# Optimization experiments

Measured on AMD Instinct MI355X. Metric: run time of the kernel, lower is better.

Reference implementation:

```python
import jax, jax.numpy as jnp
import numpy as np

D_MODEL, D_STATE, EXPAND = 256, 16, 2
D_INNER = EXPAND * D_MODEL
DT_RANK = (D_MODEL + 15) // 16
BATCH, SEQLEN = 4, 4096


def silu(x):
    return x * jax.nn.sigmoid(x)


def setup_inputs() -> dict:
    key = jax.random.key(0)
    ks = jax.random.split(key, 10)
    h = jax.random.normal(ks[0], (BATCH, SEQLEN, D_MODEL), dtype=jnp.float32)
    Wi_f = jax.random.normal(ks[1], (2 * D_INNER, D_MODEL), dtype=jnp.float32) / np.sqrt(D_MODEL)
    Wi_b = jax.random.normal(ks[2], (2 * D_INNER, D_MODEL), dtype=jnp.float32) / np.sqrt(D_MODEL)
    Wx_f = jax.random.normal(ks[3], (DT_RANK + 2 * D_STATE, D_INNER), dtype=jnp.float32) / np.sqrt(D_INNER)
    Wx_b = jax.random.normal(ks[4], (DT_RANK + 2 * D_STATE, D_INNER), dtype=jnp.float32) / np.sqrt(D_INNER)
    dt_std = DT_RANK ** -0.5
    Wdt_f = jax.random.uniform(ks[5], (D_INNER, DT_RANK), dtype=jnp.float32, minval=-dt_std, maxval=dt_std)
    Wdt_b = jax.random.uniform(ks[6], (D_INNER, DT_RANK), dtype=jnp.float32, minval=-dt_std, maxval=dt_std)
    # dt bias = inverse-softplus of dt sampled log-uniform in [1e-3, 1e-1]
    dt = jnp.exp(jax.random.uniform(ks[7], (D_INNER,), dtype=jnp.float32) * (np.log(0.1) - np.log(0.001)) + np.log(0.001))
    dt = jnp.clip(dt, 1e-4, None)
    inv_dt = dt + jnp.log(-jnp.expm1(-dt))
    bdt_f = inv_dt
    bdt_b = inv_dt
    A_log = jnp.log(jnp.broadcast_to(jnp.arange(1, D_STATE + 1, dtype=jnp.float32), (D_INNER, D_STATE)))
    A_log_f = A_log
    A_log_b = A_log
    D_f = jnp.ones((D_INNER,), dtype=jnp.float32)
    D_b = jnp.ones((D_INNER,), dtype=jnp.float32)
    Wo = jax.random.normal(ks[8], (D_MODEL, 2 * D_INNER), dtype=jnp.float32) / np.sqrt(2 * D_INNER)
    return {"hidden_states": h, "Wi_f": Wi_f, "Wi_b": Wi_b, "Wx_f": Wx_f, "Wx_b": Wx_b,
            "Wdt_f": Wdt_f, "Wdt_b": Wdt_b, "bdt_f": bdt_f, "bdt_b": bdt_b,
            "A_log_f": A_log_f, "A_log_b": A_log_b, "D_f": D_f, "D_b": D_b, "Wo": Wo}


def mamba_dir(h, Wi, Wx, Wdt, bdt, A_log, Dp, reverse):
    b, l, _ = h.shape
    di, r = Wdt.shape
    n = A_log.shape[1]
    xz = h @ Wi.T                      # [b,l,2*di]
    if reverse:
        xz = xz[:, ::-1]
    x, z = xz[..., :di], xz[..., di:]
    u = silu(x)                        # selective_scan input u
    x_dbl = u @ Wx.T                   # [b,l,r+2n]
    delta = jax.nn.softplus(x_dbl[..., :r] @ Wdt.T + bdt)   # [b,l,di]
    Bm = x_dbl[..., r:r + n]           # [b,l,n]
    Cm = x_dbl[..., r + n:r + 2 * n]   # [b,l,n]
    A = -jnp.exp(A_log)                # [di,n]

    def step(s, inp):
        u_t, d_t, B_t, C_t = inp       # [b,di],[b,di],[b,n],[b,n]
        dA = jnp.exp(d_t[..., None] * A)                         # [b,di,n]
        s = dA * s + (d_t * u_t)[..., None] * B_t[:, None, :]    # [b,di,n]
        y_t = jnp.einsum('bdn,bn->bd', s, C_t)
        return s, y_t

    s0 = jnp.zeros((b, di, n), dtype=u.dtype)
    xs = (jnp.swapaxes(u, 0, 1), jnp.swapaxes(delta, 0, 1),
          jnp.swapaxes(Bm, 0, 1), jnp.swapaxes(Cm, 0, 1))
    _, ys = jax.lax.scan(step, s0, xs)
    y = jnp.swapaxes(ys, 0, 1) + u * Dp          # skip term D*u
    y = y * silu(z)                              # gated output
    if reverse:
        y = y[:, ::-1]
    return y


def reference(hidden_states, Wi_f, Wi_b, Wx_f, Wx_b, Wdt_f, Wdt_b, bdt_f, bdt_b, A_log_f, A_log_b, D_f, D_b, Wo):
    y_f = mamba_dir(hidden_states, Wi_f, Wx_f, Wdt_f, bdt_f, A_log_f, D_f, False)
    y_b = mamba_dir(hidden_states, Wi_b, Wx_b, Wdt_b, bdt_b, A_log_b, D_b, True)
    y = jnp.concatenate([y_f, y_b], axis=-1)     # [b,l,2*di]
    return y @ Wo.T                              # [b,l,d_model]
```

## Files before the change

### kernel.cpp

```cpp
#include <hip/hip_runtime.h>
#include <hip/hip_bf16.h>
#include <cstddef>
#include <cstdint>

#define D_MODELc 256
#define D_STATEc 16
#define D_INNERc 512
#define DT_RANKc 16
#define BATCHc   4
#define SEQLENc  4096
#define NCHUNK   128
#define CHUNK    32

typedef unsigned short u16;
typedef __attribute__((ext_vector_type(8))) short bf16x8;
typedef __attribute__((ext_vector_type(4))) float f32x4;
typedef float __attribute__((ext_vector_type(4))) f4v;
typedef __attribute__((ext_vector_type(4))) uint32_t u32x4;

#define VMCNT8() asm volatile("s_waitcnt vmcnt(8)" ::: "memory")
#define VMCNT0() asm volatile("s_waitcnt vmcnt(0)" ::: "memory")

__device__ __forceinline__ float siluf(float v) { return v / (1.f + __expf(-v)); }

__device__ __forceinline__ u16 bf16_rne(float f) {
    uint32_t u = __float_as_uint(f);
    u += 0x7fffu + ((u >> 16) & 1u);
    return (u16)(u >> 16);
}
__device__ __forceinline__ float bf16_to_f(u16 h) {
    return __uint_as_float(((uint32_t)h) << 16);
}
__device__ __forceinline__ uint32_t pack_hl(float f) {
    u16 hh = bf16_rne(f);
    u16 ll = bf16_rne(f - bf16_to_f(hh));
    return ((uint32_t)hh << 16) | ll;
}
__device__ __forceinline__ float unpack_add(uint32_t v) {
    return __uint_as_float(v & 0xFFFF0000u) + __uint_as_float(v << 16);
}
__device__ __forceinline__ void unpack_frag(const uint32_t* q, bf16x8& fh, bf16x8& fl) {
    union { bf16x8 v; uint32_t w[4]; } H, L;
    #pragma unroll
    for (int i = 0; i < 4; i++) {
        uint32_t a = q[2 * i], b = q[2 * i + 1];
        H.w[i] = (a >> 16) | (b & 0xFFFF0000u);
        L.w[i] = (a & 0xFFFFu) | (b << 16);
    }
    fh = H.v; fl = L.v;
}
__device__ __forceinline__ float softplusf(float x) {
    return fmaxf(x, 0.f) + __logf(1.f + __expf(-fabsf(x)));
}
__device__ __forceinline__ float dot16_tree(const f4v x[4], const float* w, float bias) {
    float t0 = fmaf(x[0][1], w[1],  x[0][0] * w[0]);
    float t1 = fmaf(x[0][3], w[3],  x[0][2] * w[2]);
    float t2 = fmaf(x[1][1], w[5],  x[1][0] * w[4]);
    float t3 = fmaf(x[1][3], w[7],  x[1][2] * w[6]);
    float t4 = fmaf(x[2][1], w[9],  x[2][0] * w[8]);
    float t5 = fmaf(x[2][3], w[11], x[2][2] * w[10]);
    float t6 = fmaf(x[3][1], w[13], x[3][0] * w[12]);
    float t7 = fmaf(x[3][3], w[15], x[3][2] * w[14]);
    return bias + (((t0 + t1) + (t2 + t3)) + ((t4 + t5) + (t6 + t7)));
}
__device__ __forceinline__ void qladder(float q, float* qd) {
    float q2 = q * q;
    float q4 = q2 * q2;
    float q8 = q4 * q4;
    qd[0] = q;        qd[1] = q2;       qd[2] = q2 * q;     qd[3] = q4;
    qd[4] = q4 * q;   qd[5] = q4 * q2;  qd[6] = q4 * qd[2]; qd[7] = q8;
    qd[8] = q8 * q;   qd[9] = q8 * q2;  qd[10] = q8 * qd[2]; qd[11] = q8 * q4;
    qd[12] = q8 * qd[4]; qd[13] = q8 * qd[5]; qd[14] = q8 * qd[6]; qd[15] = q8 * q8;
}

#define GLL16(g, l) __builtin_amdgcn_global_load_lds( \
    (const __attribute__((address_space(1))) uint32_t*)(g), \
    (__attribute__((address_space(3))) uint32_t*)(l), 16, 0, 0)

__global__ __launch_bounds__(256) void split5_kernel(
        const float* __restrict__ s0, const float* __restrict__ s1,
        const float* __restrict__ s2, const float* __restrict__ s3,
        const float* __restrict__ s4,
        u16* __restrict__ h0, u16* __restrict__ l0,
        u16* __restrict__ h1, u16* __restrict__ l1,
        u16* __restrict__ h2, u16* __restrict__ l2,
        u16* __restrict__ h3, u16* __restrict__ l3,
        u16* __restrict__ h4, u16* __restrict__ l4,
        int n4w, int n4x) {
    const int which = blockIdx.y;
    const float* in; u16* hi; u16* lo; int n4;
    if      (which == 0) { in = s0; hi = h0; lo = l0; n4 = n4w; }
    else if (which == 1) { in = s1; hi = h1; lo = l1; n4 = n4w; }
    else if (which == 2) { in = s2; hi = h2; lo = l2; n4 = n4w; }
    else if (which == 3) { in = s3; hi = h3; lo = l3; n4 = n4x; }
    else                 { in = s4; hi = h4; lo = l4; n4 = n4x; }
    for (int i = blockIdx.x * 256 + threadIdx.x; i < n4; i += gridDim.x * 256) {
        float4 v = ((const float4*)in)[i];
        u16 a0 = bf16_rne(v.x), a1 = bf16_rne(v.y), a2 = bf16_rne(v.z), a3 = bf16_rne(v.w);
        ushort4 hv; hv.x = a0; hv.y = a1; hv.z = a2; hv.w = a3;
        ushort4 lv;
        lv.x = bf16_rne(v.x - bf16_to_f(a0));
        lv.y = bf16_rne(v.y - bf16_to_f(a1));
        lv.z = bf16_rne(v.z - bf16_to_f(a2));
        lv.w = bf16_rne(v.w - bf16_to_f(a3));
        ((ushort4*)hi)[i] = hv;
        ((ushort4*)lo)[i] = lv;
    }
}

__global__ __launch_bounds__(256) void split_kernel(const float* __restrict__ in,
                                                    u16* __restrict__ hi,
                                                    u16* __restrict__ lo, int n4) {
    int i = blockIdx.x * 256 + threadIdx.x;
    const int stride = gridDim.x * 256;
    for (; i < n4; i += stride) {
        float4 v = ((const float4*)in)[i];
        u16 a0 = bf16_rne(v.x), a1 = bf16_rne(v.y), a2 = bf16_rne(v.z), a3 = bf16_rne(v.w);
        ushort4 hv; hv.x = a0; hv.y = a1; hv.z = a2; hv.w = a3;
        ushort4 lv;
        lv.x = bf16_rne(v.x - bf16_to_f(a0));
        lv.y = bf16_rne(v.y - bf16_to_f(a1));
        lv.z = bf16_rne(v.z - bf16_to_f(a2));
        lv.w = bf16_rne(v.w - bf16_to_f(a3));
        ((ushort4*)hi)[i] = hv;
        ((ushort4*)lo)[i] = lv;
    }
}

template<int EPI, int NBL2, int AINT>
__global__ __launch_bounds__(256) void gemm_mfma(
        const u16* __restrict__ Ah, const u16* __restrict__ Al, int lda,
        const u16* __restrict__ Bh, const u16* __restrict__ Bl, int ldb,
        float* __restrict__ out0,
        uint32_t* __restrict__ uhl,
        int M, int N, int K) {
    __shared__ char lds[2][32768];
    const int t    = threadIdx.x;
    const int lane = t & 63;
    const int wid  = t >> 6;
    const int wrow = wid >> 1, wcol = wid & 1;

    const int id  = blockIdx.x;
    const int xcd = id & 7;
    const int j   = id >> 3;
    const int nb  = j & ((1 << NBL2) - 1);
    const int mg  = j >> NBL2;
    const int m0  = (mg * 8 + xcd) * 128;
    const int n0  = nb * 128;

    const int lr  = lane & 15;
    const int kgl = lane >> 4;

    f32x4 acc[4][4] = {};

    const char* gp[8];
    if (AINT == 0) {
        #pragma unroll
        for (int i = 0; i < 8; i++) {
            int c    = i * 256 + t;
            int tile = c >> 9;
            int kg   = (c >> 7) & 3;
            int row  = c & 127;
            const u16* bsrc = (tile == 0) ? Ah : (tile == 1) ? Al : (tile == 2) ? Bh : Bl;
            int r0 = (tile < 2) ? m0 : n0;
            int ld = (tile < 2) ? lda : ldb;
            gp[i] = (const char*)(bsrc + (size_t)(r0 + row) * ld + kg * 8);
        }
    } else {
        #pragma unroll
        for (int i = 0; i < 4; i++) {
            int c    = i * 256 + t;
            int kg   = c >> 8;
            int row  = (c >> 1) & 127;
            int half = c & 1;
            gp[i] = (const char*)((const uint32_t*)Ah + (size_t)(m0 + row) * lda + kg * 8 + half * 4);
        }
        #pragma unroll
        for (int i = 4; i < 8; i++) {
            int cb   = (i - 4) * 256 + t;
            int tile = cb >> 9;
            int kg   = (cb >> 7) & 3;
            int row  = cb & 127;
            const u16* bsrc = tile ? Bl : Bh;
            gp[i] = (const char*)(bsrc + (size_t)(n0 + row) * ldb + kg * 8);
        }
    }
    const int ldst_t = t << 4;

    auto stage = [&](int buf) {
        #pragma unroll
        for (int i = 0; i < 8; i++) {
            GLL16(gp[i], ((char*)lds) + buf * 32768 + i * 4096 + ldst_t);
            gp[i] += (AINT == 1 && i < 4) ? 128 : 64;
        }
    };

    const int NT = K >> 5;
    stage(0);
    if (NT > 1) stage(1);

    for (int kt = 0; kt < NT; ++kt) {
        const int buf = kt & 1;
        if (kt + 1 < NT) { VMCNT8(); } else { VMCNT0(); }
        __builtin_amdgcn_sched_barrier(0);
        __builtin_amdgcn_s_barrier();
        __builtin_amdgcn_sched_barrier(0);

        bf16x8 afh[4], afl[4];
        if (AINT == 0) {
            const u16* lb = (const u16*)lds[buf];
            #pragma unroll
            for (int mi = 0; mi < 4; mi++) {
                int row = wrow * 64 + mi * 16 + lr;
                afh[mi] = *(const bf16x8*)(lb + 0 * 4096 + kgl * 1024 + row * 8);
                afl[mi] = *(const bf16x8*)(lb + 1 * 4096 + kgl * 1024 + row * 8);
            }
        } else {
            const uint32_t* la = (const uint32_t*)lds[buf];
            #pragma unroll
            for (int mi = 0; mi < 4; mi++) {
                int row = wrow * 64 + mi * 16 + lr;
                unpack_frag(la + kgl * 1024 + row * 8, afh[mi], afl[mi]);
            }
        }
        const u16* lbB = (const u16*)(lds[buf] + 16384);
        #pragma unroll
        for (int ni = 0; ni < 4; ni++) {
            int row = wcol * 64 + ni * 16 + lr;
            bf16x8 bfh = *(const bf16x8*)(lbB + 0 * 4096 + kgl * 1024 + row * 8);
            bf16x8 bfl = *(const bf16x8*)(lbB + 1 * 4096 + kgl * 1024 + row * 8);
            #pragma unroll
            for (int mi = 0; mi < 4; mi++) {
                acc[mi][ni] = __builtin_amdgcn_mfma_f32_16x16x32_bf16(afh[mi], bfh, acc[mi][ni], 0, 0, 0);
                acc[mi][ni] = __builtin_amdgcn_mfma_f32_16x16x32_bf16(afh[mi], bfl, acc[mi][ni], 0, 0, 0);
                acc[mi][ni] = __builtin_amdgcn_mfma_f32_16x16x32_bf16(afl[mi], bfh, acc[mi][ni], 0, 0, 0);
            }
        }
        __builtin_amdgcn_sched_barrier(0);
        __builtin_amdgcn_s_barrier();
        __builtin_amdgcn_sched_barrier(0);
        if (kt + 2 < NT) stage(buf);
    }

    uint32_t* lds32 = (uint32_t*)lds;
    {
        const int dirn = (EPI == 1) ? (nb >> 3) : 0;
        const bool is_u = (EPI == 1) && (((nb >> 2) & 1) == 0);
        #pragma unroll
        for (int mi = 0; mi < 4; mi++) {
            #pragma unroll
            for (int ni = 0; ni < 4; ni++) {
                #pragma unroll
                for (int r = 0; r < 4; r++) {
                    int row = wrow * 64 + mi * 16 + kgl * 4 + r;
                    int col = wcol * 64 + ni * 16 + lr;
                    int swz = ((row >> 2) & 3) << 4;
                    float v = acc[mi][ni][r];
                    uint32_t w;
                    if (EPI == 0) w = __float_as_uint(v);
                    else {
                        float s = siluf(v);
                        w = is_u ? pack_hl(s) : __float_as_uint(s);
                    }
                    lds32[row * 128 + (col ^ swz)] = w;
                }
            }
        }
        __syncthreads();
        if (EPI == 0) {
            float* base = out0 + (size_t)m0 * N + n0;
            #pragma unroll
            for (int i = 0; i < 16; i++) {
                int idx = i * 256 + t;
                int row = idx >> 5, c4 = idx & 31;
                int swz = ((row >> 2) & 3) << 4;
                f4v v = *(const f4v*)(lds32 + row * 128 + ((c4 * 4) ^ swz));
                __builtin_nontemporal_store(v, (f4v*)(base + (size_t)row * N + c4 * 4));
            }
        } else {
            const int colbase = (nb & 3) * 128;
            if (is_u) {
                uint32_t* base = uhl + (size_t)dirn * M * 512 + (size_t)m0 * 512 + colbase;
                #pragma unroll
                for (int i = 0; i < 16; i++) {
                    int idx = i * 256 + t;
                    int row = idx >> 5, c4 = idx & 31;
                    int swz = ((row >> 2) & 3) << 4;
                    *(u32x4*)(base + (size_t)row * 512 + c4 * 4) =
                        *(const u32x4*)(lds32 + row * 128 + ((c4 * 4) ^ swz));
                }
            } else {
                float* base = out0 + (size_t)m0 * 1024 + (size_t)dirn * 512 + colbase;
                #pragma unroll
                for (int i = 0; i < 16; i++) {
                    int idx = i * 256 + t;
                    int row = idx >> 5, c4 = idx & 31;
                    int swz = ((row >> 2) & 3) << 4;
                    *(f4v*)(base + (size_t)row * 1024 + c4 * 4) =
                        *(const f4v*)(lds32 + row * 128 + ((c4 * 4) ^ swz));
                }
            }
        }
    }
}

__global__ __launch_bounds__(256) void xdbl_mfma(
        const uint32_t* __restrict__ Uhl,
        const u16* __restrict__ WxH, const u16* __restrict__ WxL,
        float* __restrict__ out) {
    __shared__ uint32_t lds[4][64][8];
    const int t    = threadIdx.x;
    const int lane = t & 63;
    const int wid  = t >> 6;
    const int m0   = blockIdx.x * 64;
    const int dir  = blockIdx.y;
    const int Mp   = gridDim.x * 64;
    const int lr   = lane & 15;
    const int kgl  = lane >> 4;

    const size_t dofU = (size_t)dir * (size_t)Mp * 512;
    const size_t dofW = (size_t)dir * (size_t)48 * 512;

    const char* gp[2];
    #pragma unroll
    for (int i = 0; i < 2; i++) {
        int c    = i * 256 + t;
        int kg   = c >> 7;
        int row  = (c >> 1) & 63;
        int half = c & 1;
        gp[i] = (const char*)(Uhl + dofU + (size_t)(m0 + row) * 512 + kg * 8 + half * 4);
    }
    const int ldst_t = t << 4;

    f32x4 acc[3] = {};

    for (int k0 = 0; k0 < 512; k0 += 32) {
        #pragma unroll
        for (int i = 0; i < 2; i++) {
            GLL16(gp[i], ((char*)lds) + i * 4096 + ldst_t);
            gp[i] += 128;
        }
        __syncthreads();

        bf16x8 afh, afl;
        unpack_frag(&lds[kgl][wid * 16 + lr][0], afh, afl);
        #pragma unroll
        for (int nf = 0; nf < 3; nf++) {
            const size_t boff = dofW + (size_t)(nf * 16 + lr) * 512 + k0 + kgl * 8;
            bf16x8 bfh = *(const bf16x8*)(WxH + boff);
            bf16x8 bfl = *(const bf16x8*)(WxL + boff);
            acc[nf] = __builtin_amdgcn_mfma_f32_16x16x32_bf16(afh, bfh, acc[nf], 0, 0, 0);
            acc[nf] = __builtin_amdgcn_mfma_f32_16x16x32_bf16(afh, bfl, acc[nf], 0, 0, 0);
            acc[nf] = __builtin_amdgcn_mfma_f32_16x16x32_bf16(afl, bfh, acc[nf], 0, 0, 0);
        }
        __syncthreads();
    }

    float* o = out + (size_t)dir * (size_t)Mp * 48;
    #pragma unroll
    for (int nf = 0; nf < 3; nf++) {
        #pragma unroll
        for (int r = 0; r < 4; r++) {
            int m = m0 + wid * 16 + kgl * 4 + r;
            int n = nf * 16 + lr;
            o[(size_t)m * 48 + n] = acc[nf][r];
        }
    }
}

__global__ __launch_bounds__(256) void scan_phaseA(
        const uint32_t* __restrict__ Uhl,
        const float* __restrict__ XD,
        const float* __restrict__ Wdt_f, const float* __restrict__ Wdt_b,
        const float* __restrict__ bdt_f, const float* __restrict__ bdt_b,
        const float* __restrict__ AL_f, const float* __restrict__ AL_b,
        float* __restrict__ SDL, float* __restrict__ S) {
    const int c   = blockIdx.x;
    const int d   = blockIdx.y * 256 + threadIdx.x;
    const int z   = blockIdx.z;
    const int dir = z & 1;
    const int b   = z >> 1;
    const int PB  = gridDim.z >> 1;
    const int Mp  = PB * SEQLENc;
    const float* Wdt = dir ? Wdt_b : Wdt_f;
    const float* bdt = dir ? bdt_b : bdt_f;
    const float* AL  = dir ? AL_b  : AL_f;
    const uint32_t* UD = Uhl + (size_t)dir * Mp * 512;
    const float* XDD = XD + (size_t)dir * Mp * 48;

    float w[16], a[16], s[16];
    #pragma unroll
    for (int n = 0; n < 16; n++) {
        w[n] = Wdt[d * 16 + n];
        a[n] = -__expf(AL[d * 16 + n]);
        s[n] = 0.f;
    }
    const float a0 = a[0];
    bool pw = (a0 != 0.f);
    #pragma unroll
    for (int n = 1; n < 16; n++)
        pw = pw && (fabsf(a[n] - (float)(n + 1) * a0) <= 3e-6f * fabsf(a[n]));
    const float bb = bdt[d];
    float sdl = 0.f;

    for (int i = 0; i < CHUNK; i++) {
        int tt = c * CHUNK + i;
        int l  = dir ? (SEQLENc - 1 - tt) : tt;
        size_t row = (size_t)b * SEQLENc + l;
        float uu = unpack_add(UD[row * 512 + d]);
        const f4v* xr4 = (const f4v*)&XDD[row * 48];
        f4v xw[4] = {xr4[0], xr4[1], xr4[2], xr4[3]};
        float dl = softplusf(dot16_tree(xw, w, bb));
        sdl += dl;
        float du = dl * uu;
        if (pw) {
            float qd[16];
            qladder(__expf(a0 * dl), qd);
            #pragma unroll
            for (int g = 0; g < 4; g++) {
                f4v B4 = xr4[4 + g];
                #pragma unroll
                for (int jj = 0; jj < 4; jj++) {
                    int n = g * 4 + jj;
                    s[n] = fmaf(qd[n], s[n], du * B4[jj]);
                }
            }
        } else {
            #pragma unroll
            for (int g = 0; g < 4; g++) {
                f4v B4 = xr4[4 + g];
                #pragma unroll
                for (int jj = 0; jj < 4; jj++) {
                    int n = g * 4 + jj;
                    float dA = __expf(dl * a[n]);
                    s[n] = fmaf(dA, s[n], du * B4[jj]);
                }
            }
        }
    }
    SDL[((size_t)z * NCHUNK + c) * 512 + d] = sdl;
    size_t base = (((size_t)z * NCHUNK + c) * 16) * 512 + d;
    #pragma unroll
    for (int n = 0; n < 16; n++)
        S[base + (size_t)n * 512] = s[n];
}

__global__ __launch_bounds__(256) void scan_phaseB(const float* __restrict__ SDL,
                                                   float* __restrict__ S,
                                                   const float* __restrict__ AL_f,
                                                   const float* __restrict__ AL_b) {
    const int g   = blockIdx.x * 256 + threadIdx.x;
    const int d   = g & 511;
    const int n   = (g >> 9) & 15;
    const int z   = g >> 13;
    const int dir = z & 1;
    const float an = -__expf((dir ? AL_b : AL_f)[d * 16 + n]);
    const size_t strideS = (size_t)16 * 512;
    size_t offS = (((size_t)z * NCHUNK) * 16 + n) * 512 + d;
    size_t offD = ((size_t)z * NCHUNK) * 512 + d;
    float carry = 0.f;
    float sdl = SDL[offD], ss = S[offS];
    for (int c = 0; c < NCHUNK; c++) {
        float sdn = 0.f, sn = 0.f;
        if (c + 1 < NCHUNK) { sdn = SDL[offD + 512]; sn = S[offS + strideS]; }
        float pp = __expf(an * sdl);
        S[offS] = carry;
        carry = pp * carry + ss;
        sdl = sdn; ss = sn;
        offS += strideS; offD += 512;
    }
}

__global__ __launch_bounds__(256) void scan_phaseC(
        const uint32_t* __restrict__ Uhl,
        const float* __restrict__ XD,
        const float* __restrict__ Wdt_f, const float* __restrict__ Wdt_b,
        const float* __restrict__ bdt_f, const float* __restrict__ bdt_b,
        const float* __restrict__ AL_f, const float* __restrict__ AL_b,
        const float* __restrict__ E,
        const float* SZ,
        const float* __restrict__ D_f,  const float* __restrict__ D_b,
        uint32_t* Yhl) {
    const int c   = blockIdx.x;
    const int d   = blockIdx.y * 256 + threadIdx.x;
    const int z   = blockIdx.z;
    const int dir = z & 1;
    const int b   = z >> 1;
    const int PB  = gridDim.z >> 1;
    const int Mp  = PB * SEQLENc;
    const float* Wdt = dir ? Wdt_b : Wdt_f;
    const float* bdt = dir ? bdt_b : bdt_f;
    const float* AL  = dir ? AL_b  : AL_f;
    const uint32_t* UD = Uhl + (size_t)dir * Mp * 512;
    const float* XDD = XD + (size_t)dir * Mp * 48;

    float w[16], a[16], s[16];
    size_t base = (((size_t)z * NCHUNK + c) * 16) * 512 + d;
    #pragma unroll
    for (int n = 0; n < 16; n++) {
        w[n] = Wdt[d * 16 + n];
        a[n] = -__expf(AL[d * 16 + n]);
        s[n] = E[base + (size_t)n * 512];
    }
    const float a0 = a[0];
    bool pw = (a0 != 0.f);
    #pragma unroll
    for (int n = 1; n < 16; n++)
        pw = pw && (fabsf(a[n] - (float)(n + 1) * a0) <= 3e-6f * fabsf(a[n]));
    const float bb = bdt[d];
    const float Dd = (dir ? D_b : D_f)[d];

    for (int i = 0; i < CHUNK; i++) {
        int tt = c * CHUNK + i;
        int l  = dir ? (SEQLENc - 1 - tt) : tt;
        size_t row = (size_t)b * SEQLENc + l;
        float uu = unpack_add(UD[row * 512 + d]);
        const f4v* xr4 = (const f4v*)&XDD[row * 48];
        f4v xw[4] = {xr4[0], xr4[1], xr4[2], xr4[3]};
        float dl = softplusf(dot16_tree(xw, w, bb));
        float du = dl * uu;
        float yp0 = 0.f, yp1 = 0.f, yp2 = 0.f, yp3 = 0.f;
        if (pw) {
            float qd[16];
            qladder(__expf(a0 * dl), qd);
            #pragma unroll
            for (int g = 0; g < 4; g++) {
                f4v B4 = xr4[4 + g];
                f4v C4 = xr4[8 + g];
                float yp = 0.f;
                #pragma unroll
                for (int jj = 0; jj < 4; jj++) {
                    int n = g * 4 + jj;
                    s[n] = fmaf(qd[n], s[n], du * B4[jj]);
                    yp = fmaf(s[n], C4[jj], yp);
                }
                if (g == 0) yp0 = yp; else if (g == 1) yp1 = yp;
                else if (g == 2) yp2 = yp; else yp3 = yp;
            }
        } else {
            #pragma unroll
            for (int g = 0; g < 4; g++) {
                f4v B4 = xr4[4 + g];
                f4v C4 = xr4[8 + g];
                float yp = 0.f;
                #pragma unroll
                for (int jj = 0; jj < 4; jj++) {
                    int n = g * 4 + jj;
                    float dA = __expf(dl * a[n]);
                    s[n] = fmaf(dA, s[n], du * B4[jj]);
                    yp = fmaf(s[n], C4[jj], yp);
                }
                if (g == 0) yp0 = yp; else if (g == 1) yp1 = yp;
                else if (g == 2) yp2 = yp; else yp3 = yp;
            }
        }
        float y = (yp0 + yp1) + (yp2 + yp3);
        size_t zi = row * 1024 + (size_t)dir * 512 + d;
        float sz = SZ[zi];
        float yv = (y + uu * Dd) * sz;
        Yhl[zi] = pack_hl(yv);
    }
}

extern "C" void kernel_launch(void* const* d_in, const int* in_sizes, int n_in,
                              void* d_out, int out_size, void* d_ws, size_t ws_size,
                              hipStream_t stream) {
    const float* h    = (const float*)d_in[0];
    const float* Wi_f = (const float*)d_in[1];
    const float* Wi_b = (const float*)d_in[2];
    const float* Wx_f = (const float*)d_in[3];
    const float* Wx_b = (const float*)d_in[4];
    const float* Wdt_f= (const float*)d_in[5];
    const float* Wdt_b= (const float*)d_in[6];
    const float* bdt_f= (const float*)d_in[7];
    const float* bdt_b= (const float*)d_in[8];
    const float* Al_f = (const float*)d_in[9];
    const float* Al_b = (const float*)d_in[10];
    const float* D_f  = (const float*)d_in[11];
    const float* D_b  = (const float*)d_in[12];
    const float* Wo   = (const float*)d_in[13];
    float* out = (float*)d_out;

    const size_t W_ELE  = 1024 * 256;
    const size_t WX_ELE = 48 * 512;
    const size_t FB   = (size_t)SEQLENc * D_INNERc;
    const size_t FH   = (size_t)SEQLENc * D_MODELc;
    const size_t FX   = (size_t)SEQLENc * 48;
    const size_t FP   = (size_t)NCHUNK * 16 * 512;
    const size_t FD   = (size_t)NCHUNK * 512;

    const size_t fixed_bytes = (8 * W_ELE + 4 * WX_ELE) * sizeof(u16);
    const size_t per_b = 2 * FH * sizeof(u16)
                       + 2 * FB * sizeof(float)
                       + 2 * FB * sizeof(uint32_t)
                       + 2 * FX * sizeof(float)
                       + 2 * (FP + FD) * sizeof(float);
    int PB = 4;
    if (fixed_bytes + 4 * per_b + 65536 > ws_size) PB = 2;
    if (fixed_bytes + 2 * per_b + 65536 > ws_size) PB = 1;

    char* cur = (char*)d_ws;
    auto alloc = [&](size_t bytes) -> char* {
        char* p = cur; cur += (bytes + 255) & ~(size_t)255; return p;
    };
    u16* WiH = (u16*)alloc(2 * W_ELE * 2);
    u16* WiL = (u16*)alloc(2 * W_ELE * 2);
    u16* WoH = (u16*)alloc(W_ELE * 2);
    u16* WoL = (u16*)alloc(W_ELE * 2);
    u16* WxH = (u16*)alloc(2 * WX_ELE * 2);
    u16* WxL = (u16*)alloc(2 * WX_ELE * 2);
    u16*      hH  = (u16*)alloc((size_t)PB * FH * 2);
    u16*      hL  = (u16*)alloc((size_t)PB * FH * 2);
    float*    sz  = (float*)alloc((size_t)PB * 2 * FB * 4);
    uint32_t* uhl = (uint32_t*)alloc((size_t)PB * 2 * FB * 4);
    float*    xd  = (float*)alloc((size_t)PB * 2 * FX * 4);
    float*    SDL = (float*)alloc((size_t)PB * 2 * FD * 4);
    float*    S   = (float*)alloc((size_t)PB * 2 * FP * 4);
    uint32_t* yhl = (uint32_t*)sz;

    {
        int n4w = (int)(W_ELE / 4);
        int n4x = (int)(WX_ELE / 4);
        split5_kernel<<<dim3(64, 5), 256, 0, stream>>>(
            Wi_f, Wi_b, Wo, Wx_f, Wx_b,
            WiH, WiL, WiH + W_ELE, WiL + W_ELE, WoH, WoL,
            WxH, WxL, WxH + WX_ELE, WxL + WX_ELE,
            n4w, n4x);
    }

    for (int b0 = 0; b0 < BATCHc; b0 += PB) {
        const int Mp = PB * SEQLENc;
        const int MB = Mp / 128;
        const float* hB = h   + (size_t)b0 * FH;
        float*       oB = out + (size_t)b0 * FH;

        {
            int n4 = (int)((size_t)PB * FH / 4);
            int blocks = (n4 + 255) / 256; if (blocks > 2048) blocks = 2048;
            split_kernel<<<blocks, 256, 0, stream>>>(hB, hH, hL, n4);
        }

        gemm_mfma<1, 4, 0><<<16 * MB, 256, 0, stream>>>(
            hH, hL, D_MODELc, WiH, WiL, D_MODELc,
            sz, uhl, Mp, 2048, D_MODELc);

        xdbl_mfma<<<dim3(Mp / 64, 2), 256, 0, stream>>>(uhl, WxH, WxL, xd);

        scan_phaseA<<<dim3(NCHUNK, 2, 2 * PB), 256, 0, stream>>>(
            uhl, xd, Wdt_f, Wdt_b, bdt_f, bdt_b, Al_f, Al_b, SDL, S);
        scan_phaseB<<<PB * 64, 256, 0, stream>>>(SDL, S, Al_f, Al_b);
        scan_phaseC<<<dim3(NCHUNK, 2, 2 * PB), 256, 0, stream>>>(
            uhl, xd, Wdt_f, Wdt_b, bdt_f, bdt_b, Al_f, Al_b,
            S, sz, D_f, D_b, yhl);

        gemm_mfma<0, 1, 1><<<2 * MB, 256, 0, stream>>>(
            (const u16*)yhl, nullptr, 1024, WoH, WoL, 1024,
            oB, nullptr, Mp, D_MODELc, 1024);
    }
}
```

Before: 317.5 us.

## Process two M-tiles per block in input GEMM and split-K the output GEMM

The input projection GEMM now has each block handle two consecutive 128-row M tiles with a continuous load pipeline, so the shared B (weight) tiles stay cache-hot and launch/prologue cost is amortized. The output projection GEMM is split along K into two halves to double the grid and improve occupancy. The second half writes into a new partial buffer, and an added elementwise kernel sums it into the output. This costs an extra full-output read/write pass, a second launch and a second accumulator array, which raises register pressure.

```diff
diff --git a/kernel.cpp b/kernel.cpp
--- a/kernel.cpp
+++ b/kernel.cpp
@@ -127,7 +127,18 @@
     }
 }
 
-template<int EPI, int NBL2, int AINT>
+__global__ __launch_bounds__(256) void add_kernel(float* __restrict__ out,
+                                                  const float* __restrict__ part,
+                                                  int n4) {
+    int i = blockIdx.x * 256 + threadIdx.x;
+    for (; i < n4; i += gridDim.x * 256) {
+        f4v a = ((const f4v*)out)[i];
+        f4v b = ((const f4v*)part)[i];
+        ((f4v*)out)[i] = a + b;
+    }
+}
+
+template<int EPI, int NBL2, int AINT, int MTILES, int KSPLIT>
 __global__ __launch_bounds__(256) void gemm_mfma(
         const u16* __restrict__ Ah, const u16* __restrict__ Al, int lda,
         const u16* __restrict__ Bh, const u16* __restrict__ Bl, int ldb,
@@ -144,14 +155,19 @@
     const int xcd = id & 7;
     const int j   = id >> 3;
     const int nb  = j & ((1 << NBL2) - 1);
-    const int mg  = j >> NBL2;
-    const int m0  = (mg * 8 + xcd) * 128;
+    const int jj  = j >> NBL2;
+    const int ks  = (KSPLIT == 2) ? (jj & 1) : 0;
+    const int mg  = (KSPLIT == 2) ? (jj >> 1) : jj;
+    const int m0  = (mg * 8 + xcd) * (128 * MTILES);
     const int n0  = nb * 128;
+    const int Keff  = K / KSPLIT;
+    const int kbase = ks * Keff;
 
     const int lr  = lane & 15;
     const int kgl = lane >> 4;
 
-    f32x4 acc[4][4] = {};
+    f32x4 acc0[4][4] = {};
+    f32x4 acc1[4][4] = {};
 
     const char* gp[8];
     if (AINT == 0) {
@@ -164,7 +180,7 @@
             const u16* bsrc = (tile == 0) ? Ah : (tile == 1) ? Al : (tile == 2) ? Bh : Bl;
             int r0 = (tile < 2) ? m0 : n0;
             int ld = (tile < 2) ? lda : ldb;
-            gp[i] = (const char*)(bsrc + (size_t)(r0 + row) * ld + kg * 8);
+            gp[i] = (const char*)(bsrc + (size_t)(r0 + row) * ld + kg * 8 + kbase);
         }
     } else {
         #pragma unroll
@@ -173,7 +189,7 @@
             int kg   = c >> 8;
             int row  = (c >> 1) & 127;
             int half = c & 1;
-            gp[i] = (const char*)((const uint32_t*)Ah + (size_t)(m0 + row) * lda + kg * 8 + half * 4);
+            gp[i] = (const char*)((const uint32_t*)Ah + (size_t)(m0 + row) * lda + kg * 8 + half * 4 + kbase);
         }
         #pragma unroll
         for (int i = 4; i < 8; i++) {
@@ -182,7 +198,7 @@
             int kg   = (cb >> 7) & 3;
             int row  = cb & 127;
             const u16* bsrc = tile ? Bl : Bh;
-            gp[i] = (const char*)(bsrc + (size_t)(n0 + row) * ldb + kg * 8);
+            gp[i] = (const char*)(bsrc + (size_t)(n0 + row) * ldb + kg * 8 + kbase);
         }
     }
     const int ldst_t = t << 4;
@@ -195,17 +211,7 @@
         }
     };
 
-    const int NT = K >> 5;
-    stage(0);
-    if (NT > 1) stage(1);
-
-    for (int kt = 0; kt < NT; ++kt) {
-        const int buf = kt & 1;
-        if (kt + 1 < NT) { VMCNT8(); } else { VMCNT0(); }
-        __builtin_amdgcn_sched_barrier(0);
-        __builtin_amdgcn_s_barrier();
-        __builtin_amdgcn_sched_barrier(0);
-
+    auto compute = [&](int buf, f32x4 (&acc)[4][4]) {
         bf16x8 afh[4], afl[4];
         if (AINT == 0) {
             const u16* lb = (const u16*)lds[buf];
@@ -236,14 +242,50 @@
                 acc[mi][ni] = __builtin_amdgcn_mfma_f32_16x16x32_bf16(afl[mi], bfh, acc[mi][ni], 0, 0, 0);
             }
         }
+    };
+
+    const int NT = Keff >> 5;
+    stage(0);
+    stage(1);
+
+    for (int kt = 0; kt < NT; ++kt) {
+        const int buf = kt & 1;
+        if (MTILES == 2 || kt + 1 < NT) { VMCNT8(); } else { VMCNT0(); }
         __builtin_amdgcn_sched_barrier(0);
         __builtin_amdgcn_s_barrier();
         __builtin_amdgcn_sched_barrier(0);
-        if (kt + 2 < NT) stage(buf);
-    }
-
-    uint32_t* lds32 = (uint32_t*)lds;
-    {
+        compute(buf, acc0);
+        __builtin_amdgcn_sched_barrier(0);
+        __builtin_amdgcn_s_barrier();
+        __builtin_amdgcn_sched_barrier(0);
+        int g = kt + 2;
+        if (MTILES == 2 && g == NT) {
+            if (AINT == 0) {
+                #pragma unroll
+                for (int i = 0; i < 4; i++) gp[i] += (size_t)128 * lda * 2 - (size_t)Keff * 2;
+                #pragma unroll
+                for (int i = 4; i < 8; i++) gp[i] -= (size_t)Keff * 2;
+            }
+        }
+        if (g < MTILES * NT) stage(g & 1);
+    }
+    if constexpr (MTILES == 2) {
+        for (int kt = NT; kt < 2 * NT; ++kt) {
+            const int buf = kt & 1;
+            if (kt + 1 < 2 * NT) { VMCNT8(); } else { VMCNT0(); }
+            __builtin_amdgcn_sched_barrier(0);
+            __builtin_amdgcn_s_barrier();
+            __builtin_amdgcn_sched_barrier(0);
+            compute(buf, acc1);
+            __builtin_amdgcn_sched_barrier(0);
+            __builtin_amdgcn_s_barrier();
+            __builtin_amdgcn_sched_barrier(0);
+            if (kt + 2 < 2 * NT) stage(kt & 1);
+        }
+    }
+
+    auto epilog = [&](f32x4 (&acc)[4][4], int mbase) {
+        uint32_t* lds32 = (uint32_t*)lds;
         const int dirn = (EPI == 1) ? (nb >> 3) : 0;
         const bool is_u = (EPI == 1) && (((nb >> 2) & 1) == 0);
         #pragma unroll
@@ -268,19 +310,20 @@
         }
         __syncthreads();
         if (EPI == 0) {
-            float* base = out0 + (size_t)m0 * N + n0;
+            float* obase = (KSPLIT == 2 && ks == 1) ? (float*)uhl : out0;
+            float* base = obase + (size_t)mbase * N + n0;
             #pragma unroll
             for (int i = 0; i < 16; i++) {
                 int idx = i * 256 + t;
                 int row = idx >> 5, c4 = idx & 31;
                 int swz = ((row >> 2) & 3) << 4;
-                f4v v = *(const f4v*)(lds32 + row * 128 + ((c4 * 4) ^ swz));
-                __builtin_nontemporal_store(v, (f4v*)(base + (size_t)row * N + c4 * 4));
+                *(f4v*)(base + (size_t)row * N + c4 * 4) =
+                    *(const f4v*)(lds32 + row * 128 + ((c4 * 4) ^ swz));
             }
         } else {
             const int colbase = (nb & 3) * 128;
             if (is_u) {
-                uint32_t* base = uhl + (size_t)dirn * M * 512 + (size_t)m0 * 512 + colbase;
+                uint32_t* base = uhl + (size_t)dirn * M * 512 + (size_t)mbase * 512 + colbase;
                 #pragma unroll
                 for (int i = 0; i < 16; i++) {
                     int idx = i * 256 + t;
@@ -290,7 +333,7 @@
                         *(const u32x4*)(lds32 + row * 128 + ((c4 * 4) ^ swz));
                 }
             } else {
-                float* base = out0 + (size_t)m0 * 1024 + (size_t)dirn * 512 + colbase;
+                float* base = out0 + (size_t)mbase * 1024 + (size_t)dirn * 512 + colbase;
                 #pragma unroll
                 for (int i = 0; i < 16; i++) {
                     int idx = i * 256 + t;
@@ -301,6 +344,11 @@
                 }
             }
         }
+    };
+    epilog(acc0, m0);
+    if constexpr (MTILES == 2) {
+        __syncthreads();
+        epilog(acc1, m0 + 128);
     }
 }
 
@@ -594,7 +642,8 @@
                        + 2 * FB * sizeof(float)
                        + 2 * FB * sizeof(uint32_t)
                        + 2 * FX * sizeof(float)
-                       + 2 * (FP + FD) * sizeof(float);
+                       + 2 * (FP + FD) * sizeof(float)
+                       + FH * sizeof(float);
     int PB = 4;
     if (fixed_bytes + 4 * per_b + 65536 > ws_size) PB = 2;
     if (fixed_bytes + 2 * per_b + 65536 > ws_size) PB = 1;
@@ -616,6 +665,7 @@
     float*    xd  = (float*)alloc((size_t)PB * 2 * FX * 4);
     float*    SDL = (float*)alloc((size_t)PB * 2 * FD * 4);
     float*    S   = (float*)alloc((size_t)PB * 2 * FP * 4);
+    float*    part1 = (float*)alloc((size_t)PB * FH * 4);
     uint32_t* yhl = (uint32_t*)sz;
 
     {
@@ -640,7 +690,7 @@
             split_kernel<<<blocks, 256, 0, stream>>>(hB, hH, hL, n4);
         }
 
-        gemm_mfma<1, 4, 0><<<16 * MB, 256, 0, stream>>>(
+        gemm_mfma<1, 4, 0, 2, 1><<<16 * (MB / 2), 256, 0, stream>>>(
             hH, hL, D_MODELc, WiH, WiL, D_MODELc,
             sz, uhl, Mp, 2048, D_MODELc);
 
@@ -653,8 +703,9 @@
             uhl, xd, Wdt_f, Wdt_b, bdt_f, bdt_b, Al_f, Al_b,
             S, sz, D_f, D_b, yhl);
 
-        gemm_mfma<0, 1, 1><<<2 * MB, 256, 0, stream>>>(
+        gemm_mfma<0, 1, 1, 1, 2><<<4 * MB, 256, 0, stream>>>(
             (const u16*)yhl, nullptr, 1024, WoH, WoL, 1024,
-            oB, nullptr, Mp, D_MODELc, 1024);
-    }
-}
+            oB, (uint32_t*)part1, Mp, D_MODELc, 1024);
+        add_kernel<<<1024, 256, 0, stream>>>(oB, part1, Mp * D_MODELc / 4);
+    }
+}
```

Result: slower. 330.3 us (+4.0%).
